# Performance work log

Measured on AMD Instinct MI355X. Metric: run time of the kernel, lower is better.

The kernel has to match this reference:

```python
import jax, jax.numpy as jnp
import numpy as np

# Repo globals / config
VOCAB_SIZE = 14
TOK_DIM = 8
POS_DIM = 8
D_MODEL = TOK_DIM + POS_DIM  # 16
MAX_SEQ_LEN = 2048
N_HEADS = 2
HEAD_DIM = 3
ATTN_DIM = N_HEADS * HEAD_DIM  # 6
FFN_DIM = 3
B, T = 16, 2048
EPS = 1e-5


def _ln(x, w, b):
    m = jnp.mean(x, axis=-1, keepdims=True)
    v = jnp.var(x, axis=-1, keepdims=True)
    return (x - m) * jax.lax.rsqrt(v + EPS) * w + b


def setup_inputs() -> dict:
    key = jax.random.key(0)
    ks = jax.random.split(key, 20)
    g = lambda k, shape: (jax.random.normal(k, shape, jnp.float32) * 0.1)
    return {
        "idx": jax.random.randint(ks[0], (B, T), 0, VOCAB_SIZE),
        "tok_emb": g(ks[1], (VOCAB_SIZE, TOK_DIM)),
        "pos_enc": g(ks[2], (MAX_SEQ_LEN, POS_DIM)),
        "Wq": g(ks[3], (ATTN_DIM, POS_DIM)),
        "Wk": g(ks[4], (ATTN_DIM, POS_DIM)),
        "Wv": g(ks[5], (ATTN_DIM, TOK_DIM)),
        "Wo": g(ks[6], (D_MODEL, ATTN_DIM)),
        "ln1_w": jnp.ones((D_MODEL,), jnp.float32),
        "ln1_b": jnp.zeros((D_MODEL,), jnp.float32),
        "ln2_w": jnp.ones((D_MODEL,), jnp.float32),
        "ln2_b": jnp.zeros((D_MODEL,), jnp.float32),
        "lnf_w": jnp.ones((D_MODEL,), jnp.float32),
        "lnf_b": jnp.zeros((D_MODEL,), jnp.float32),
        "W1": g(ks[7], (FFN_DIM, D_MODEL)),
        "b1": jnp.zeros((FFN_DIM,), jnp.float32),
        "W2": g(ks[8], (D_MODEL, FFN_DIM)),
        "b2": jnp.zeros((D_MODEL,), jnp.float32),
        "Wh": g(ks[9], (TOK_DIM, D_MODEL)),
    }


def reference(idx, tok_emb, pos_enc, Wq, Wk, Wv, Wo,
              ln1_w, ln1_b, ln2_w, ln2_b, lnf_w, lnf_b,
              W1, b1, W2, b2, Wh):
    Bq, Tq = idx.shape
    tok = tok_emb[idx]                                  # [B,T,TOK_DIM]
    pos = jnp.broadcast_to(pos_enc[:Tq][None], (Bq, Tq, POS_DIM))
    x = jnp.concatenate([tok, pos], axis=-1)            # [B,T,D_MODEL]
    h = _ln(x, ln1_w, ln1_b)
    x_tok = h[..., :TOK_DIM]
    x_pos = h[..., TOK_DIM:]
    # projections (torch Linear: y = x @ W.T)
    q = (x_pos @ Wq.T).reshape(Bq, Tq, N_HEADS, HEAD_DIM).transpose(0, 2, 1, 3)
    k = (x_pos @ Wk.T).reshape(Bq, Tq, N_HEADS, HEAD_DIM).transpose(0, 2, 1, 3)
    v = (x_tok @ Wv.T).reshape(Bq, Tq, N_HEADS, HEAD_DIM).transpose(0, 2, 1, 3)
    scores = jnp.einsum('bhqd,bhkd->bhqk', q, k) / jnp.sqrt(jnp.float32(HEAD_DIM))
    mask = jnp.tril(jnp.ones((Tq, Tq), dtype=bool))
    scores = jnp.where(mask[None, None], scores, -jnp.inf)
    attn = jax.nn.softmax(scores, axis=-1)
    out = jnp.einsum('bhqk,bhkd->bhqd', attn, v)
    out = out.transpose(0, 2, 1, 3).reshape(Bq, Tq, ATTN_DIM)
    x = x + out @ Wo.T
    h2 = _ln(x, ln2_w, ln2_b)
    x = x + (jax.nn.gelu(h2 @ W1.T + b1, approximate=False) @ W2.T + b2)
    x = _ln(x, lnf_w, lnf_b)
    return (x @ Wh.T) @ tok_emb.T                       # tied head -> [B,T,VOCAB]
```

## Files before the change

kernel.cpp:

```cpp
#include <hip/hip_runtime.h>
#include <math.h>

#define BB    16
#define TT    2048
#define VOCAB 14
#define TOKD  8
#define POSD  8
#define DM    16
#define NH    2
#define HD    3
#define AD    6
#define FFND  3

#define NTOK  (BB*TT)
#define BH    (BB*NH)
#define TPB   36
#define NTILE (BH*TPB)

struct P {
    const int*   idx;
    const float* tok_emb;
    const float* pos_enc;
    const float* Wq;
    const float* Wk;
    const float* Wv;
    const float* Wo;
    const float* ln1w;
    const float* ln1b;
    const float* ln2w;
    const float* ln2b;
    const float* lnfw;
    const float* lnfb;
    const float* W1;
    const float* b1;
    const float* W2;
    const float* b2;
    const float* Wh;
    float*       out;
    float4*      qbuf;
    float4*      kvf;
    float4*      pbuf;
};

__global__ __launch_bounds__(256) void prep_kernel(P p) {
    int gid = blockIdx.x * 256 + threadIdx.x;
    if (gid >= NTOK) return;
    int t = gid & (TT - 1);
    int b = gid >> 11;

    float x[DM];
    int tok = p.idx[gid];
    #pragma unroll
    for (int j = 0; j < TOKD; ++j) x[j]        = p.tok_emb[tok * TOKD + j];
    #pragma unroll
    for (int j = 0; j < POSD; ++j) x[TOKD + j] = p.pos_enc[t * POSD + j];

    float m = 0.f;
    #pragma unroll
    for (int j = 0; j < DM; ++j) m += x[j];
    m *= (1.f / DM);
    float v = 0.f;
    #pragma unroll
    for (int j = 0; j < DM; ++j) { float d = x[j] - m; v += d * d; }
    v *= (1.f / DM);
    float rs = rsqrtf(v + 1e-5f);
    float h[DM];
    #pragma unroll
    for (int j = 0; j < DM; ++j)
        h[j] = (x[j] - m) * rs * p.ln1w[j] + p.ln1b[j];

    float q[AD], k[AD], vv[AD];
    #pragma unroll
    for (int a = 0; a < AD; ++a) {
        float sq = 0.f, sk = 0.f, sv = 0.f;
        #pragma unroll
        for (int j = 0; j < 8; ++j) {
            sq = fmaf(p.Wq[a * 8 + j], h[TOKD + j], sq);
            sk = fmaf(p.Wk[a * 8 + j], h[TOKD + j], sk);
            sv = fmaf(p.Wv[a * 8 + j], h[j], sv);
        }
        q[a] = sq; k[a] = sk; vv[a] = sv;
    }

    const float QS = 1.4426950408889634f / 1.7320508075688772f;
    #pragma unroll
    for (int hh = 0; hh < NH; ++hh) {
        size_t base = (size_t)(b * NH + hh) * TT + t;
        p.qbuf[base] = make_float4(q[hh*3] * QS, q[hh*3+1] * QS, q[hh*3+2] * QS, 0.f);
        p.kvf[base * 2]     = make_float4(k[hh*3],  k[hh*3+1],  k[hh*3+2],  0.f);
        p.kvf[base * 2 + 1] = make_float4(vv[hh*3], vv[hh*3+1], vv[hh*3+2], 0.f);
    }
}

#define LOADKV(it)                                                             \
    float4 Kr = skv[((kw + (it)) << 1)];                                       \
    float4 Vr = skv[((kw + (it)) << 1) + 1];                                   \
    float k0 = Kr.x, k1 = Kr.y, k2 = Kr.z;                                     \
    float v0 = Vr.x, v1 = Vr.y, v2 = Vr.z;

__global__ __launch_bounds__(256) void attn_kernel(P p) {
    __shared__ float4 skv[512];
    __shared__ float4 sq[256];
    __shared__ float4 spart[1024];

    const int tid  = threadIdx.x;
    int tile = blockIdx.x;
    int bh   = tile / TPB;
    int r    = tile - bh * TPB;
    int s    = 0;
    while (((s + 1) * (s + 2)) / 2 <= r) ++s;
    int c    = r - (s * (s + 1)) / 2;

    const float4* kvsrc = p.kvf + ((size_t)bh * TT + (c << 8)) * 2;
    skv[tid]       = kvsrc[tid];
    skv[256 + tid] = kvsrc[256 + tid];
    sq [tid] = p.qbuf[(size_t)bh * TT + (s << 8) + tid];
    __syncthreads();

    int wv   = tid >> 6;
    int lane = tid & 63;
    int kw   = wv << 6;

    float4 qr[4];
    #pragma unroll
    for (int j = 0; j < 4; ++j) qr[j] = sq[(j << 6) + lane];

    float ac[4][4];
    #pragma unroll
    for (int j = 0; j < 4; ++j)
        ac[j][0] = ac[j][1] = ac[j][2] = ac[j][3] = 0.f;

    if (c < s) {
        #pragma unroll 4
        for (int it = 0; it < 64; ++it) {
            LOADKV(it)
            #pragma unroll
            for (int j = 0; j < 4; ++j) {
                float sc = fmaf(qr[j].x, k0, fmaf(qr[j].y, k1, qr[j].z * k2));
                float pr = __builtin_amdgcn_exp2f(sc);
                ac[j][0] = fmaf(pr, v0, ac[j][0]);
                ac[j][1] = fmaf(pr, v1, ac[j][1]);
                ac[j][2] = fmaf(pr, v2, ac[j][2]);
                ac[j][3] += pr;
            }
        }
    } else {
        #pragma unroll
        for (int j = 0; j < 4; ++j) {
            if (j < wv) continue;
            if (j == wv) {
                #pragma unroll 4
                for (int it = 0; it < 64; ++it) {
                    LOADKV(it)
                    float sc = fmaf(qr[j].x, k0, fmaf(qr[j].y, k1, qr[j].z * k2));
                    float pr = __builtin_amdgcn_exp2f(sc);
                    pr = (it <= lane) ? pr : 0.f;
                    ac[j][0] = fmaf(pr, v0, ac[j][0]);
                    ac[j][1] = fmaf(pr, v1, ac[j][1]);
                    ac[j][2] = fmaf(pr, v2, ac[j][2]);
                    ac[j][3] += pr;
                }
            } else {
                #pragma unroll 4
                for (int it = 0; it < 64; ++it) {
                    LOADKV(it)
                    float sc = fmaf(qr[j].x, k0, fmaf(qr[j].y, k1, qr[j].z * k2));
                    float pr = __builtin_amdgcn_exp2f(sc);
                    ac[j][0] = fmaf(pr, v0, ac[j][0]);
                    ac[j][1] = fmaf(pr, v1, ac[j][1]);
                    ac[j][2] = fmaf(pr, v2, ac[j][2]);
                    ac[j][3] += pr;
                }
            }
        }
    }

    #pragma unroll
    for (int j = 0; j < 4; ++j)
        spart[(wv << 8) + (j << 6) + lane] =
            make_float4(ac[j][0], ac[j][1], ac[j][2], ac[j][3]);
    __syncthreads();

    float4 p0 = spart[tid];
    float4 p1 = spart[256 + tid];
    float4 p2 = spart[512 + tid];
    float4 p3 = spart[768 + tid];
    float4 acc = make_float4(p0.x+p1.x+p2.x+p3.x, p0.y+p1.y+p2.y+p3.y,
                             p0.z+p1.z+p2.z+p3.z, p0.w+p1.w+p2.w+p3.w);
    p.pbuf[((size_t)bh * 8 + c) * TT + (s << 8) + tid] = acc;
}

__global__ __launch_bounds__(256) void epi_kernel(P p) {
    int gid = blockIdx.x * 256 + threadIdx.x;
    if (gid >= NTOK) return;
    int t = gid & (TT - 1);
    int b = gid >> 11;
    int s = t >> 8;

    float x[DM];
    int tok = p.idx[gid];
    #pragma unroll
    for (int j = 0; j < TOKD; ++j) x[j]        = p.tok_emb[tok * TOKD + j];
    #pragma unroll
    for (int j = 0; j < POSD; ++j) x[TOKD + j] = p.pos_enc[t * POSD + j];

    float att[AD];
    #pragma unroll
    for (int hh = 0; hh < NH; ++hh) {
        const float4* pp = p.pbuf + ((size_t)(b * NH + hh) * 8) * TT + t;
        float4 acc = pp[0];
        for (int c = 1; c <= s; ++c) {
            float4 e = pp[(size_t)c * TT];
            acc.x += e.x; acc.y += e.y; acc.z += e.z; acc.w += e.w;
        }
        float inv = 1.f / acc.w;
        att[hh*3+0] = acc.x * inv;
        att[hh*3+1] = acc.y * inv;
        att[hh*3+2] = acc.z * inv;
    }

    float xo[DM];
    #pragma unroll
    for (int j = 0; j < DM; ++j) {
        float sacc = x[j];
        #pragma unroll
        for (int a = 0; a < AD; ++a) sacc = fmaf(p.Wo[j * AD + a], att[a], sacc);
        xo[j] = sacc;
    }

    float m = 0.f;
    #pragma unroll
    for (int j = 0; j < DM; ++j) m += xo[j];
    m *= (1.f / DM);
    float v = 0.f;
    #pragma unroll
    for (int j = 0; j < DM; ++j) { float d = xo[j] - m; v += d * d; }
    v *= (1.f / DM);
    float rs = rsqrtf(v + 1e-5f);
    float h2[DM];
    #pragma unroll
    for (int j = 0; j < DM; ++j)
        h2[j] = (xo[j] - m) * rs * p.ln2w[j] + p.ln2b[j];

    float g[FFND];
    #pragma unroll
    for (int cc = 0; cc < FFND; ++cc) {
        float f = p.b1[cc];
        #pragma unroll
        for (int j = 0; j < DM; ++j) f = fmaf(p.W1[cc * DM + j], h2[j], f);
        g[cc] = 0.5f * f * (1.f + erff(f * 0.70710678118654752f));
    }
    float x2[DM];
    #pragma unroll
    for (int j = 0; j < DM; ++j) {
        float sacc = xo[j] + p.b2[j];
        #pragma unroll
        for (int cc = 0; cc < FFND; ++cc) sacc = fmaf(p.W2[j * FFND + cc], g[cc], sacc);
        x2[j] = sacc;
    }

    m = 0.f;
    #pragma unroll
    for (int j = 0; j < DM; ++j) m += x2[j];
    m *= (1.f / DM);
    v = 0.f;
    #pragma unroll
    for (int j = 0; j < DM; ++j) { float d = x2[j] - m; v += d * d; }
    v *= (1.f / DM);
    rs = rsqrtf(v + 1e-5f);
    float y[DM];
    #pragma unroll
    for (int j = 0; j < DM; ++j)
        y[j] = (x2[j] - m) * rs * p.lnfw[j] + p.lnfb[j];

    float t8[TOKD];
    #pragma unroll
    for (int pp = 0; pp < TOKD; ++pp) {
        float sacc = 0.f;
        #pragma unroll
        for (int j = 0; j < DM; ++j) sacc = fmaf(p.Wh[pp * DM + j], y[j], sacc);
        t8[pp] = sacc;
    }
    float* op = p.out + (size_t)gid * VOCAB;
    #pragma unroll
    for (int vcb = 0; vcb < VOCAB; ++vcb) {
        float sacc = 0.f;
        #pragma unroll
        for (int pp = 0; pp < TOKD; ++pp)
            sacc = fmaf(t8[pp], p.tok_emb[vcb * TOKD + pp], sacc);
        op[vcb] = sacc;
    }
}

extern "C" void kernel_launch(void* const* d_in, const int* in_sizes, int n_in,
                              void* d_out, int out_size, void* d_ws, size_t ws_size,
                              hipStream_t stream) {
    P p;
    p.idx     = (const int*)d_in[0];
    p.tok_emb = (const float*)d_in[1];
    p.pos_enc = (const float*)d_in[2];
    p.Wq      = (const float*)d_in[3];
    p.Wk      = (const float*)d_in[4];
    p.Wv      = (const float*)d_in[5];
    p.Wo      = (const float*)d_in[6];
    p.ln1w    = (const float*)d_in[7];
    p.ln1b    = (const float*)d_in[8];
    p.ln2w    = (const float*)d_in[9];
    p.ln2b    = (const float*)d_in[10];
    p.lnfw    = (const float*)d_in[11];
    p.lnfb    = (const float*)d_in[12];
    p.W1      = (const float*)d_in[13];
    p.b1      = (const float*)d_in[14];
    p.W2      = (const float*)d_in[15];
    p.b2      = (const float*)d_in[16];
    p.Wh      = (const float*)d_in[17];
    p.out     = (float*)d_out;
    p.qbuf    = (float4*)d_ws;
    p.kvf     = (float4*)((char*)d_ws + (1u << 20));
    p.pbuf    = (float4*)((char*)d_ws + (3u << 20));

    prep_kernel<<<NTOK / 256, 256, 0, stream>>>(p);
    attn_kernel<<<NTILE, 256, 0, stream>>>(p);
    epi_kernel<<<NTOK / 256, 256, 0, stream>>>(p);
}
```

Before: 128.4 us.

## Use 512-query by 256-key attention tiles to double K/V reuse per block

Each attention block now handles 512 queries (8 per thread) against one 256-key chunk, not 256 queries. Each K/V value loaded from shared memory is reused across twice as many queries, and the grid shrinks from 36 to 20 tiles per head. Diagonal tiles use a masked loop, and the upper-half tile starts at query group 4 so fully masked work is skipped. In exchange the kernel uses more registers (32 accumulators plus 24 query values) and more shared memory, which may lower occupancy, and the grid is smaller.

```diff
diff --git a/kernel.cpp b/kernel.cpp
--- a/kernel.cpp
+++ b/kernel.cpp
@@ -14,8 +14,8 @@
 
 #define NTOK  (BB*TT)
 #define BH    (BB*NH)
-#define TPB   36
-#define NTILE (BH*TPB)
+#define TPB2  20
+#define NTILE2 (BH*TPB2)
 
 struct P {
     const int*   idx;
@@ -92,102 +92,85 @@
     }
 }
 
-#define LOADKV(it)                                                             \
-    float4 Kr = skv[((kw + (it)) << 1)];                                       \
-    float4 Vr = skv[((kw + (it)) << 1) + 1];                                   \
-    float k0 = Kr.x, k1 = Kr.y, k2 = Kr.z;                                     \
-    float v0 = Vr.x, v1 = Vr.y, v2 = Vr.z;
-
 __global__ __launch_bounds__(256) void attn_kernel(P p) {
     __shared__ float4 skv[512];
-    __shared__ float4 sq[256];
-    __shared__ float4 spart[1024];
+    __shared__ float4 spart[2048];
 
     const int tid  = threadIdx.x;
     int tile = blockIdx.x;
-    int bh   = tile / TPB;
-    int r    = tile - bh * TPB;
+    int bh   = tile / TPB2;
+    int r    = tile - bh * TPB2;
     int s    = 0;
-    while (((s + 1) * (s + 2)) / 2 <= r) ++s;
-    int c    = r - (s * (s + 1)) / 2;
+    while ((s + 1) * (s + 2) <= r) ++s;
+    int c    = r - s * (s + 1);
+    int dpar = c - 2 * s;
 
     const float4* kvsrc = p.kvf + ((size_t)bh * TT + (c << 8)) * 2;
     skv[tid]       = kvsrc[tid];
     skv[256 + tid] = kvsrc[256 + tid];
-    sq [tid] = p.qbuf[(size_t)bh * TT + (s << 8) + tid];
-    __syncthreads();
 
     int wv   = tid >> 6;
     int lane = tid & 63;
-    int kw   = wv << 6;
-
-    float4 qr[4];
-    #pragma unroll
-    for (int j = 0; j < 4; ++j) qr[j] = sq[(j << 6) + lane];
-
-    float ac[4][4];
-    #pragma unroll
-    for (int j = 0; j < 4; ++j)
+    int kb   = wv << 6;
+
+    float qx[8], qy[8], qz[8];
+    const float4* qsrc = p.qbuf + (size_t)bh * TT + ((size_t)s << 9);
+    #pragma unroll
+    for (int j = 0; j < 8; ++j) {
+        float4 q4 = qsrc[(j << 6) + lane];
+        qx[j] = q4.x; qy[j] = q4.y; qz[j] = q4.z;
+    }
+
+    float ac[8][4];
+    #pragma unroll
+    for (int j = 0; j < 8; ++j)
         ac[j][0] = ac[j][1] = ac[j][2] = ac[j][3] = 0.f;
 
-    if (c < s) {
-        #pragma unroll 4
-        for (int it = 0; it < 64; ++it) {
-            LOADKV(it)
-            #pragma unroll
-            for (int j = 0; j < 4; ++j) {
-                float sc = fmaf(qr[j].x, k0, fmaf(qr[j].y, k1, qr[j].z * k2));
-                float pr = __builtin_amdgcn_exp2f(sc);
-                ac[j][0] = fmaf(pr, v0, ac[j][0]);
-                ac[j][1] = fmaf(pr, v1, ac[j][1]);
-                ac[j][2] = fmaf(pr, v2, ac[j][2]);
-                ac[j][3] += pr;
-            }
+    __syncthreads();
+
+    #define KLOOP(J0, MASKED, KOFF)                                           \
+        _Pragma("unroll 2")                                                   \
+        for (int it = 0; it < 64; ++it) {                                     \
+            float4 Kr = skv[(kb + it) << 1];                                  \
+            float4 Vr = skv[((kb + it) << 1) + 1];                            \
+            float k0 = Kr.x, k1 = Kr.y, k2 = Kr.z;                            \
+            float v0 = Vr.x, v1 = Vr.y, v2 = Vr.z;                            \
+            int keyloc = (KOFF) + kb + it;                                    \
+            _Pragma("unroll")                                                 \
+            for (int j = (J0); j < 8; ++j) {                                  \
+                float sc = fmaf(qx[j], k0, fmaf(qy[j], k1, qz[j] * k2));      \
+                float pr = __builtin_amdgcn_exp2f(sc);                        \
+                if (MASKED) pr = (keyloc <= ((j << 6) + lane)) ? pr : 0.f;    \
+                ac[j][0] = fmaf(pr, v0, ac[j][0]);                            \
+                ac[j][1] = fmaf(pr, v1, ac[j][1]);                            \
+                ac[j][2] = fmaf(pr, v2, ac[j][2]);                            \
+                ac[j][3] += pr;                                               \
+            }                                                                 \
         }
-    } else {
-        #pragma unroll
-        for (int j = 0; j < 4; ++j) {
-            if (j < wv) continue;
-            if (j == wv) {
-                #pragma unroll 4
-                for (int it = 0; it < 64; ++it) {
-                    LOADKV(it)
-                    float sc = fmaf(qr[j].x, k0, fmaf(qr[j].y, k1, qr[j].z * k2));
-                    float pr = __builtin_amdgcn_exp2f(sc);
-                    pr = (it <= lane) ? pr : 0.f;
-                    ac[j][0] = fmaf(pr, v0, ac[j][0]);
-                    ac[j][1] = fmaf(pr, v1, ac[j][1]);
-                    ac[j][2] = fmaf(pr, v2, ac[j][2]);
-                    ac[j][3] += pr;
-                }
-            } else {
-                #pragma unroll 4
-                for (int it = 0; it < 64; ++it) {
-                    LOADKV(it)
-                    float sc = fmaf(qr[j].x, k0, fmaf(qr[j].y, k1, qr[j].z * k2));
-                    float pr = __builtin_amdgcn_exp2f(sc);
-                    ac[j][0] = fmaf(pr, v0, ac[j][0]);
-                    ac[j][1] = fmaf(pr, v1, ac[j][1]);
-                    ac[j][2] = fmaf(pr, v2, ac[j][2]);
-                    ac[j][3] += pr;
-                }
-            }
-        }
-    }
-
-    #pragma unroll
-    for (int j = 0; j < 4; ++j)
-        spart[(wv << 8) + (j << 6) + lane] =
+
+    if (dpar < 0)      { KLOOP(0, false, 0)   }
+    else if (dpar == 0){ KLOOP(0, true,  0)   }
+    else               { KLOOP(4, true,  256) }
+
+    #undef KLOOP
+
+    #pragma unroll
+    for (int j = 0; j < 8; ++j)
+        spart[(wv << 9) + (j << 6) + lane] =
             make_float4(ac[j][0], ac[j][1], ac[j][2], ac[j][3]);
     __syncthreads();
 
-    float4 p0 = spart[tid];
-    float4 p1 = spart[256 + tid];
-    float4 p2 = spart[512 + tid];
-    float4 p3 = spart[768 + tid];
-    float4 acc = make_float4(p0.x+p1.x+p2.x+p3.x, p0.y+p1.y+p2.y+p3.y,
-                             p0.z+p1.z+p2.z+p3.z, p0.w+p1.w+p2.w+p3.w);
-    p.pbuf[((size_t)bh * 8 + c) * TT + (s << 8) + tid] = acc;
+    #pragma unroll
+    for (int o = 0; o < 512; o += 256) {
+        int slot = o + tid;
+        float4 a0 = spart[slot];
+        float4 a1 = spart[512 + slot];
+        float4 a2 = spart[1024 + slot];
+        float4 a3 = spart[1536 + slot];
+        float4 acc = make_float4(a0.x+a1.x+a2.x+a3.x, a0.y+a1.y+a2.y+a3.y,
+                                 a0.z+a1.z+a2.z+a3.z, a0.w+a1.w+a2.w+a3.w);
+        p.pbuf[((size_t)bh * 8 + c) * TT + ((size_t)s << 9) + slot] = acc;
+    }
 }
 
 __global__ __launch_bounds__(256) void epi_kernel(P p) {
@@ -320,6 +303,6 @@
     p.pbuf    = (float4*)((char*)d_ws + (3u << 20));
 
     prep_kernel<<<NTOK / 256, 256, 0, stream>>>(p);
-    attn_kernel<<<NTILE, 256, 0, stream>>>(p);
+    attn_kernel<<<NTILE2, 256, 0, stream>>>(p);
     epi_kernel<<<NTOK / 256, 256, 0, stream>>>(p);
 }
```

New measurement: 132.3 us. 3.0% more time.

## Fuse LN1 and QKV projection into attention kernel, drop prep kernel

Applied to the files above, without the earlier changes.

Removes the separate prep kernel and its q/k/v workspace buffers. Each attention tile now recomputes the embedding lookup, LayerNorm and Q/K/V projections for its 256 key and 256 query tokens directly into shared memory. This saves one kernel launch and the global write and read of the intermediate buffers. In exchange, LN1 and the projections are recomputed once per tile, many times per token across the triangular tile grid.

```diff
diff --git a/kernel.cpp b/kernel.cpp
--- a/kernel.cpp
+++ b/kernel.cpp
@@ -37,19 +37,12 @@
     const float* b2;
     const float* Wh;
     float*       out;
-    float4*      qbuf;
-    float4*      kvf;
     float4*      pbuf;
 };
 
-__global__ __launch_bounds__(256) void prep_kernel(P p) {
-    int gid = blockIdx.x * 256 + threadIdx.x;
-    if (gid >= NTOK) return;
-    int t = gid & (TT - 1);
-    int b = gid >> 11;
-
+__device__ __forceinline__ void ln1_of(const P& p, int b, int t, float* h) {
     float x[DM];
-    int tok = p.idx[gid];
+    int tok = p.idx[b * TT + t];
     #pragma unroll
     for (int j = 0; j < TOKD; ++j) x[j]        = p.tok_emb[tok * TOKD + j];
     #pragma unroll
@@ -64,32 +57,9 @@
     for (int j = 0; j < DM; ++j) { float d = x[j] - m; v += d * d; }
     v *= (1.f / DM);
     float rs = rsqrtf(v + 1e-5f);
-    float h[DM];
     #pragma unroll
     for (int j = 0; j < DM; ++j)
         h[j] = (x[j] - m) * rs * p.ln1w[j] + p.ln1b[j];
-
-    float q[AD], k[AD], vv[AD];
-    #pragma unroll
-    for (int a = 0; a < AD; ++a) {
-        float sq = 0.f, sk = 0.f, sv = 0.f;
-        #pragma unroll
-        for (int j = 0; j < 8; ++j) {
-            sq = fmaf(p.Wq[a * 8 + j], h[TOKD + j], sq);
-            sk = fmaf(p.Wk[a * 8 + j], h[TOKD + j], sk);
-            sv = fmaf(p.Wv[a * 8 + j], h[j], sv);
-        }
-        q[a] = sq; k[a] = sk; vv[a] = sv;
-    }
-
-    const float QS = 1.4426950408889634f / 1.7320508075688772f;
-    #pragma unroll
-    for (int hh = 0; hh < NH; ++hh) {
-        size_t base = (size_t)(b * NH + hh) * TT + t;
-        p.qbuf[base] = make_float4(q[hh*3] * QS, q[hh*3+1] * QS, q[hh*3+2] * QS, 0.f);
-        p.kvf[base * 2]     = make_float4(k[hh*3],  k[hh*3+1],  k[hh*3+2],  0.f);
-        p.kvf[base * 2 + 1] = make_float4(vv[hh*3], vv[hh*3+1], vv[hh*3+2], 0.f);
-    }
 }
 
 #define LOADKV(it)                                                             \
@@ -110,11 +80,45 @@
     int s    = 0;
     while (((s + 1) * (s + 2)) / 2 <= r) ++s;
     int c    = r - (s * (s + 1)) / 2;
-
-    const float4* kvsrc = p.kvf + ((size_t)bh * TT + (c << 8)) * 2;
-    skv[tid]       = kvsrc[tid];
-    skv[256 + tid] = kvsrc[256 + tid];
-    sq [tid] = p.qbuf[(size_t)bh * TT + (s << 8) + tid];
+    int b    = bh >> 1;
+    int hh   = bh & 1;
+
+    {
+        float hK[DM];
+        ln1_of(p, b, (c << 8) + tid, hK);
+        float k0=0.f,k1=0.f,k2=0.f,v0=0.f,v1=0.f,v2=0.f;
+        const float* wk = p.Wk + (hh * 3) * 8;
+        const float* wv_ = p.Wv + (hh * 3) * 8;
+        #pragma unroll
+        for (int j = 0; j < 8; ++j) {
+            k0 = fmaf(wk[j],      hK[TOKD + j], k0);
+            k1 = fmaf(wk[8 + j],  hK[TOKD + j], k1);
+            k2 = fmaf(wk[16 + j], hK[TOKD + j], k2);
+            v0 = fmaf(wv_[j],      hK[j], v0);
+            v1 = fmaf(wv_[8 + j],  hK[j], v1);
+            v2 = fmaf(wv_[16 + j], hK[j], v2);
+        }
+        skv[(tid << 1)]     = make_float4(k0, k1, k2, 0.f);
+        skv[(tid << 1) + 1] = make_float4(v0, v1, v2, 0.f);
+
+        float hQ[DM];
+        if (c != s) {
+            ln1_of(p, b, (s << 8) + tid, hQ);
+        } else {
+            #pragma unroll
+            for (int j = 0; j < DM; ++j) hQ[j] = hK[j];
+        }
+        const float QS = 1.4426950408889634f / 1.7320508075688772f;
+        float q0=0.f,q1=0.f,q2=0.f;
+        const float* wq = p.Wq + (hh * 3) * 8;
+        #pragma unroll
+        for (int j = 0; j < 8; ++j) {
+            q0 = fmaf(wq[j],      hQ[TOKD + j], q0);
+            q1 = fmaf(wq[8 + j],  hQ[TOKD + j], q1);
+            q2 = fmaf(wq[16 + j], hQ[TOKD + j], q2);
+        }
+        sq[tid] = make_float4(q0 * QS, q1 * QS, q2 * QS, 0.f);
+    }
     __syncthreads();
 
     int wv   = tid >> 6;
@@ -315,11 +319,8 @@
     p.b2      = (const float*)d_in[16];
     p.Wh      = (const float*)d_in[17];
     p.out     = (float*)d_out;
-    p.qbuf    = (float4*)d_ws;
-    p.kvf     = (float4*)((char*)d_ws + (1u << 20));
-    p.pbuf    = (float4*)((char*)d_ws + (3u << 20));
-
-    prep_kernel<<<NTOK / 256, 256, 0, stream>>>(p);
+    p.pbuf    = (float4*)d_ws;
+
     attn_kernel<<<NTILE, 256, 0, stream>>>(p);
     epi_kernel<<<NTOK / 256, 256, 0, stream>>>(p);
 }
```

Measured after the change: 127.1 us. No clear change (-1.1%).
